# Kernel tuning notes

Measured on AMD Instinct MI355X. Metric: run time of the kernel, lower is better.

## Reference

```python
import jax, jax.numpy as jnp
from jax import lax
import numpy as np

N_QUBITS = 8
Q_DEPTH = 10
DIM = 256  # 2**8

# basis-state bit table; wire 0 = most-significant bit (PennyLane convention)
_bits = ((np.arange(DIM)[:, None] >> (N_QUBITS - 1 - np.arange(N_QUBITS))) & 1)
# phase layer: S on even wires (phase i), T on odd wires (phase e^{i pi/4})
_ph = np.where(np.arange(N_QUBITS) % 2 == 0, 1j, np.exp(1j * np.pi / 4))
_diag = np.prod(np.power(_ph[None, :], _bits), axis=1)
# entangling_layer_3 CZ pattern
_cz = np.ones(DIM)
for i, j in [(0, 1), (2, 3), (4, 5), (6, 7), (1, 2), (3, 4), (5, 6)]:
    _cz = _cz * ((-1.0) ** (_bits[:, i] * _bits[:, j]))
DIAG = jnp.asarray((_diag * _cz).astype(np.complex64))  # phase+CZ layer fused diagonal
ZSIGNS = jnp.asarray((1 - 2 * _bits).astype(np.float32))  # [256, 8] PauliZ eigenvalues
H_GATE = jnp.asarray((np.array([[1.0, 1.0], [1.0, -1.0]]) / np.sqrt(2.0)).astype(np.complex64))
X_GATE = jnp.asarray(np.array([[0.0, 1.0], [1.0, 0.0]]).astype(np.complex64))
EYE2 = jnp.eye(2, dtype=jnp.complex64)
BN_EPS = 1e-5


def apply_1q(state, U, w):
    """Apply 2x2 gate U on wire w; state: [B, 2,2,...,2]."""
    state = jnp.moveaxis(state, w + 1, -1)
    state = jnp.matmul(state, U.T)
    return jnp.moveaxis(state, -1, w + 1)


def quantum_net(features, q_params):
    """Batched statevector sim of quantum_net_3. features [B,256], q_params [80] -> [B,8]."""
    f = features / jnp.linalg.norm(features, axis=1, keepdims=True)
    state = f.astype(jnp.complex64).reshape((-1,) + (2,) * N_QUBITS)
    for w in range(N_QUBITS):
        state = apply_1q(state, H_GATE, w)
    qw = q_params.reshape(Q_DEPTH, N_QUBITS)
    for layer in range(Q_DEPTH):
        for w in range(N_QUBITS):
            t = qw[layer, w]
            c = jnp.cos(t / 2).astype(jnp.complex64)
            s = jnp.sin(t / 2).astype(jnp.complex64)
            U = c * EYE2 + (-1j) * s * X_GATE  # RX(t)
            state = apply_1q(state, U, w)
        flat = state.reshape(-1, DIM) * DIAG  # phase layer + CZ entangling (diagonal)
        state = flat.reshape((-1,) + (2,) * N_QUBITS)
    sv = state.reshape(-1, DIM)
    probs = sv.real ** 2 + sv.imag ** 2
    return probs @ ZSIGNS  # [B, 8] expval(PauliZ_i)


def conv2d(x, w, b):
    y = lax.conv_general_dilated(x, w, (1, 1), 'SAME', dimension_numbers=('NCHW', 'OIHW', 'NCHW'))
    return y + b[None, :, None, None]


def bn(x, gamma, beta, mean, var):  # eval-mode BatchNorm2d
    inv = gamma / jnp.sqrt(var + BN_EPS)
    return x * inv[None, :, None, None] + (beta - mean * inv)[None, :, None, None]


def maxpool2(x):
    return lax.reduce_window(x, -jnp.inf, lax.max, (1, 1, 2, 2), (1, 1, 2, 2), 'VALID')


def setup_inputs() -> dict:
    key = jax.random.key(0)
    ks = jax.random.split(key, 16)
    B = 1024
    return {
        'x': jax.random.normal(ks[0], (B, 1, 28, 28), dtype=jnp.float32),
        'conv1_w': 0.1 * jax.random.normal(ks[1], (32, 1, 3, 3), dtype=jnp.float32),
        'conv1_b': jnp.zeros((32,), jnp.float32),
        'bn1_gamma': jnp.ones((32,), jnp.float32),
        'bn1_beta': jnp.zeros((32,), jnp.float32),
        'bn1_mean': jnp.zeros((32,), jnp.float32),
        'bn1_var': jnp.ones((32,), jnp.float32),
        'conv2_w': 0.05 * jax.random.normal(ks[2], (64, 32, 3, 3), dtype=jnp.float32),
        'conv2_b': jnp.zeros((64,), jnp.float32),
        'bn2_gamma': jnp.ones((64,), jnp.float32),
        'bn2_beta': jnp.zeros((64,), jnp.float32),
        'bn2_mean': jnp.zeros((64,), jnp.float32),
        'bn2_var': jnp.ones((64,), jnp.float32),
        'fc_w': 0.01 * jax.random.normal(ks[3], (256, 64 * 7 * 7), dtype=jnp.float32),
        'fc_b': jnp.zeros((256,), jnp.float32),
        'q_params': 0.1 * jax.random.normal(ks[4], (Q_DEPTH * N_QUBITS,), dtype=jnp.float32),
        'p1_w': 0.01 * jax.random.normal(ks[5], (128, 8), dtype=jnp.float32),
        'p1_b': jnp.zeros((128,), jnp.float32),
        'p2_w': 0.01 * jax.random.normal(ks[6], (64, 128), dtype=jnp.float32),
        'p2_b': jnp.zeros((64,), jnp.float32),
        'p3_w': 0.01 * jax.random.normal(ks[7], (10, 64), dtype=jnp.float32),
        'p3_b': jnp.zeros((10,), jnp.float32),
    }


def reference(x, conv1_w, conv1_b, bn1_gamma, bn1_beta, bn1_mean, bn1_var,
              conv2_w, conv2_b, bn2_gamma, bn2_beta, bn2_mean, bn2_var,
              fc_w, fc_b, q_params, p1_w, p1_b, p2_w, p2_b, p3_w, p3_b):
    h = maxpool2(jax.nn.relu(bn(conv2d(x, conv1_w, conv1_b), bn1_gamma, bn1_beta, bn1_mean, bn1_var)))
    h = maxpool2(jax.nn.relu(bn(conv2d(h, conv2_w, conv2_b), bn2_gamma, bn2_beta, bn2_mean, bn2_var)))
    h = h.reshape(h.shape[0], -1)  # [B, 64*7*7]
    feats = jnp.tanh(h @ fc_w.T + fc_b)  # [B, 256]
    q = quantum_net(feats, q_params)  # [B, 8]
    z = jax.nn.relu(q @ p1_w.T + p1_b)  # dropout = identity (eval)
    z = jax.nn.relu(z @ p2_w.T + p2_b)
    return z @ p3_w.T + p3_b
```

## Files before the change

kernel.cpp:

```cpp
#include <hip/hip_runtime.h>
#include <math.h>


#define B_SZ 1024

#define OFF_FCWP   0
#define OFF_W2F    802816
#define OFF_W1T    821248
#define OFF_SC1    821536
#define OFF_SH1    821568
#define OFF_SC2    821600
#define OFF_SH2    821664
#define OFF_H1     821728
#define OFF_H2P    7244256

#define KSPLIT_FC 14
#define KCHUNK_FC 224

typedef __attribute__((ext_vector_type(8))) short s16x8;
typedef __attribute__((ext_vector_type(4))) float f32x4;

__constant__ float C_COS8[8] = {1.f, 0.70710678f, 0.f, -0.70710678f, -1.f, -0.70710678f, 0.f, 0.70710678f};
__constant__ float C_SIN8[8] = {0.f, 0.70710678f, 1.f, 0.70710678f, 0.f, -0.70710678f, -1.f, -0.70710678f};

__device__ __forceinline__ unsigned short bf16_rne(float f) {
  unsigned u = __float_as_uint(f);
  unsigned r = u + 0x7FFFu + ((u >> 16) & 1u);
  return (unsigned short)(r >> 16);
}
__device__ __forceinline__ int div14(int m) {
  return __float2int_rz((float)m * 0.07142858f);
}

__global__ __launch_bounds__(256) void prep_kernel(
    const float* __restrict__ fc_w, const float* __restrict__ c2w, const float* __restrict__ c1w,
    const float* __restrict__ bn1g, const float* __restrict__ bn1b, const float* __restrict__ bn1m,
    const float* __restrict__ bn1v, const float* __restrict__ c1b,
    const float* __restrict__ bn2g, const float* __restrict__ bn2b, const float* __restrict__ bn2m,
    const float* __restrict__ bn2v, const float* __restrict__ c2b,
    float* __restrict__ ws) {
  int g = blockIdx.x * 256 + threadIdx.x;

  {
    int j = g & 7, lane = (g >> 3) & 63, nt = (g >> 9) & 15, kg = g >> 13;
    int n = nt * 16 + (lane & 15);
    int k = kg * 32 + ((lane >> 4) & 3) * 8 + j;
    float v = fc_w[n * 3136 + (k & 63) * 49 + (k >> 6)];
    unsigned short hi = bf16_rne(v);
    unsigned short lo = bf16_rne(v - __uint_as_float((unsigned)hi << 16));
    unsigned short* us = (unsigned short*)ws;
    int base = ((kg * 16 + nt) * 2) * 512 + lane * 8 + j;
    us[base] = hi;
    us[base + 512] = lo;
  }

  if (g < 36864) {
    int j = g & 7, L = (g >> 3) & 63, rest = g >> 9;
    int h = rest & 1; rest >>= 1;
    int t = rest % 9, w = rest / 9;
    int occ = w * 16 + (L & 15);
    int ic  = (L >> 4) * 8 + j;
    float v = c2w[occ * 288 + ic * 9 + t];
    unsigned short hi = bf16_rne(v);
    unsigned short res = hi;
    if (h) res = bf16_rne(v - __uint_as_float((unsigned)hi << 16));
    ((unsigned short*)(ws + OFF_W2F))[g] = res;
  }
  if (g < 288) {
    ws[OFF_W1T + g] = c1w[(g & 31) * 9 + (g >> 5)];
  }
  if (g < 32) {
    float inv = bn1g[g] / sqrtf(bn1v[g] + 1e-5f);
    ws[OFF_SC1 + g] = inv;
    ws[OFF_SH1 + g] = c1b[g] * inv + bn1b[g] - bn1m[g] * inv;
  }
  if (g < 64) {
    float inv = bn2g[g] / sqrtf(bn2v[g] + 1e-5f);
    ws[OFF_SC2 + g] = inv;
    ws[OFF_SH2 + g] = c2b[g] * inv + bn2b[g] - bn2m[g] * inv;
  }
}

__global__ __launch_bounds__(256) void conv1_kernel(
    const float* __restrict__ x, const float* __restrict__ w1T,
    const float* __restrict__ sc1, const float* __restrict__ sh1,
    float* __restrict__ h1) {
  const int b = blockIdx.x, tid = threadIdx.x;
  __shared__ float xs[30][32];
  __shared__ float w1s[288];
  __shared__ float sc1s[32], sh1s[32];

  float4* xsf = (float4*)&xs[0][0];
  if (tid < 240) xsf[tid] = make_float4(0.f, 0.f, 0.f, 0.f);
  __syncthreads();
  const float* xb = x + b * 784;
  for (int i = tid; i < 784; i += 256) {
    int y = i / 28, c = i - y * 28;
    xs[y + 1][c + 1] = xb[i];
  }
  for (int i = tid; i < 288; i += 256) w1s[i] = w1T[i];
  if (tid < 32) { sc1s[tid] = sc1[tid]; sh1s[tid] = sh1[tid]; }
  __syncthreads();

  for (int t = tid; t < 448; t += 256) {
    const int oc = t & 31, py = t >> 5;
    float wv[9];
#pragma unroll
    for (int k = 0; k < 9; ++k) wv[k] = w1s[k * 32 + oc];
    float acc0[28], acc1[28];
#pragma unroll
    for (int j = 0; j < 28; ++j) { acc0[j] = 0.f; acc1[j] = 0.f; }
#pragma unroll
    for (int r = 0; r < 4; ++r) {
      const int pr = 2 * py + r;
      float row[32];
#pragma unroll
      for (int q = 0; q < 8; ++q) {
        float4 v = *(const float4*)&xs[pr][4 * q];
        row[4 * q] = v.x; row[4 * q + 1] = v.y; row[4 * q + 2] = v.z; row[4 * q + 3] = v.w;
      }
      if (r <= 2) {
#pragma unroll
        for (int kx = 0; kx < 3; ++kx) {
          const float w = wv[r * 3 + kx];
#pragma unroll
          for (int xx = 0; xx < 28; ++xx) acc0[xx] = fmaf(row[xx + kx], w, acc0[xx]);
        }
      }
      if (r >= 1) {
#pragma unroll
        for (int kx = 0; kx < 3; ++kx) {
          const float w = wv[(r - 1) * 3 + kx];
#pragma unroll
          for (int xx = 0; xx < 28; ++xx) acc1[xx] = fmaf(row[xx + kx], w, acc1[xx]);
        }
      }
    }
    const float sc = sc1s[oc], sh = sh1s[oc];
    float* dst = h1 + b * 6272 + oc * 196 + py * 14;
#pragma unroll
    for (int px = 0; px < 14; ++px) {
      float v0 = fmaxf(fmaf(acc0[2 * px], sc, sh), 0.f);
      float v1 = fmaxf(fmaf(acc0[2 * px + 1], sc, sh), 0.f);
      float v2 = fmaxf(fmaf(acc1[2 * px], sc, sh), 0.f);
      float v3 = fmaxf(fmaf(acc1[2 * px + 1], sc, sh), 0.f);
      dst[px] = fmaxf(fmaxf(v0, v1), fmaxf(v2, v3));
    }
  }
}

__global__ __launch_bounds__(256, 2) void conv2_kernel(
    const float* __restrict__ h1, const float* __restrict__ w2f_f,
    const float* __restrict__ sc2, const float* __restrict__ sh2,
    unsigned short* __restrict__ h2hi, unsigned short* __restrict__ h2lo) {
  const int b = blockIdx.x, tid = threadIdx.x;
  const int lane = tid & 63, w = tid >> 6;

  __shared__ unsigned char lds_raw[50176];
  unsigned short* tile_hi = (unsigned short*)lds_raw;
  unsigned short* tile_lo = (unsigned short*)(lds_raw + 17408);
  float* conv_out = (float*)lds_raw;

  const unsigned short* w2f = (const unsigned short*)w2f_f;
  s16x8 bf[9][2];
#pragma unroll
  for (int t = 0; t < 9; ++t)
#pragma unroll
    for (int h = 0; h < 2; ++h)
      bf[t][h] = *(const s16x8*)&w2f[(((w * 9 + t) * 2 + h) << 9) + lane * 8];

  {
    float4* z = (float4*)lds_raw;
    for (int i = tid; i < 2176; i += 256) z[i] = make_float4(0.f, 0.f, 0.f, 0.f);
  }
  __syncthreads();

  if (tid < 196) {
    const int y = div14(tid), x = tid - y * 14;
    const int sp = ((y + 1) * 16 + (x + 1)) * 32;
    const float* src = h1 + b * 6272 + tid;
#pragma unroll
    for (int c = 0; c < 4; ++c) {
      s16x8 hv, lv;
#pragma unroll
      for (int j = 0; j < 8; ++j) {
        float v = src[(c * 8 + j) * 196];
        unsigned short h16 = bf16_rne(v);
        hv[j] = (short)h16;
        lv[j] = (short)bf16_rne(v - __uint_as_float((unsigned)h16 << 16));
      }
      *(s16x8*)&tile_hi[sp + c * 8] = hv;
      *(s16x8*)&tile_lo[sp + c * 8] = lv;
    }
  }
  __syncthreads();

  f32x4 acc[13];
#pragma unroll
  for (int i = 0; i < 13; ++i) acc[i] = (f32x4){0.f, 0.f, 0.f, 0.f};

  const int kg8 = (lane >> 4) * 8;
#pragma unroll
  for (int mt = 0; mt < 13; ++mt) {
    const int m = mt * 16 + (lane & 15);
    const int y = div14(m), x = m - y * 14;
    const int base = (y * 16 + x) * 32 + kg8;
#pragma unroll
    for (int dy = 0; dy < 3; ++dy) {
#pragma unroll
      for (int dx = 0; dx < 3; ++dx) {
        const int off = base + (dy * 16 + dx) * 32;
        s16x8 ah = *(s16x8*)&tile_hi[off];
        s16x8 al = *(s16x8*)&tile_lo[off];
        const int t = dy * 3 + dx;
        acc[mt] = __builtin_amdgcn_mfma_f32_16x16x32_bf16(ah, bf[t][0], acc[mt], 0, 0, 0);
        acc[mt] = __builtin_amdgcn_mfma_f32_16x16x32_bf16(ah, bf[t][1], acc[mt], 0, 0, 0);
        acc[mt] = __builtin_amdgcn_mfma_f32_16x16x32_bf16(al, bf[t][0], acc[mt], 0, 0, 0);
      }
    }
  }
  __syncthreads();

  const int oc = w * 16 + (lane & 15);
  const float sc = sc2[oc], sh = sh2[oc];
  float* cw = conv_out + w * 3136;
#pragma unroll
  for (int mt = 0; mt < 13; ++mt) {
#pragma unroll
    for (int r = 0; r < 4; ++r) {
      const int m = mt * 16 + (lane >> 4) * 4 + r;
      if (m < 196) cw[m * 16 + (lane & 15)] = fmaxf(fmaf(acc[mt][r], sc, sh), 0.f);
    }
  }
  __syncthreads();

#pragma unroll
  for (int i = 0; i < 13; ++i) {
    const int ps = i * 4 + (lane >> 4);
    if (ps < 49) {
      const int py = (ps * 37) >> 8, px = ps - py * 7;
      const int m00 = py * 28 + px * 2;
      const int c0 = m00 * 16 + (lane & 15);
      float v0 = cw[c0], v1 = cw[c0 + 16], v2 = cw[c0 + 224], v3 = cw[c0 + 240];
      float vm = fmaxf(fmaxf(v0, v1), fmaxf(v2, v3));
      unsigned short hv = bf16_rne(vm);
      const int idx = b * 3136 + ps * 64 + oc;
      h2hi[idx] = hv;
      h2lo[idx] = bf16_rne(vm - __uint_as_float((unsigned)hv << 16));
    }
  }
}

__global__ __launch_bounds__(256) void fc_mfma_kernel(
    const unsigned short* __restrict__ h2hi, const unsigned short* __restrict__ h2lo,
    const unsigned short* __restrict__ Bfrag, float* __restrict__ Part) {
  __shared__ unsigned short Bs[8192];
  const int tid = threadIdx.x;
  const int lane = tid & 63, w = tid >> 6;
  const int m0 = blockIdx.y * 64, nt0 = blockIdx.x * 8, z = blockIdx.z;
  const int kz = z * KCHUNK_FC;

  const int mrow = m0 + w * 16 + (lane & 15);
  const int kg8 = (lane >> 4) * 8;
  const unsigned short* arow_hi = h2hi + mrow * 3136;
  const unsigned short* arow_lo = h2lo + mrow * 3136;

  f32x4 acc[8];
#pragma unroll
  for (int i = 0; i < 8; ++i) acc[i] = (f32x4){0.f, 0.f, 0.f, 0.f};

  for (int c = 0; c < 7; ++c) {
    const int kg = (kz >> 5) + c;
    {
      const uint4* src = (const uint4*)(Bfrag + (size_t)(kg * 16 + nt0) * 1024);
      uint4* dst = (uint4*)Bs;
#pragma unroll
      for (int i = 0; i < 4; ++i) dst[tid + 256 * i] = src[tid + 256 * i];
    }
    __syncthreads();

    const int k0 = kz + c * 32;
    s16x8 ah = *(const s16x8*)(arow_hi + k0 + kg8);
    s16x8 al = *(const s16x8*)(arow_lo + k0 + kg8);
#pragma unroll
    for (int nf = 0; nf < 8; ++nf) {
      s16x8 bh = *(s16x8*)&Bs[(nf * 2 + 0) * 512 + lane * 8];
      s16x8 bl = *(s16x8*)&Bs[(nf * 2 + 1) * 512 + lane * 8];
      acc[nf] = __builtin_amdgcn_mfma_f32_16x16x32_bf16(ah, bh, acc[nf], 0, 0, 0);
      acc[nf] = __builtin_amdgcn_mfma_f32_16x16x32_bf16(ah, bl, acc[nf], 0, 0, 0);
      acc[nf] = __builtin_amdgcn_mfma_f32_16x16x32_bf16(al, bh, acc[nf], 0, 0, 0);
    }
    __syncthreads();
  }

  float* dst = Part + (size_t)z * 262144;
  const int mbase = m0 + w * 16 + (lane >> 4) * 4;
  const int nbase = nt0 * 16 + (lane & 15);
#pragma unroll
  for (int nf = 0; nf < 8; ++nf) {
#pragma unroll
    for (int r = 0; r < 4; ++r) {
      dst[(mbase + r) * 256 + nbase + nf * 16] = acc[nf][r];
    }
  }
}

__global__ __launch_bounds__(256) void quantum_kernel(
    const float* __restrict__ Part, const float* __restrict__ fc_b,
    const float* __restrict__ qp,
    const float* __restrict__ p1w, const float* __restrict__ p1b,
    const float* __restrict__ p2w, const float* __restrict__ p2b,
    const float* __restrict__ p3w, const float* __restrict__ p3b,
    float* __restrict__ out) {
  const int b = blockIdx.x, tid = threadIdx.x;
  __shared__ float2 buf[2][256];
  __shared__ float csl[160];
  __shared__ float part[4][8];
  __shared__ float qv[8];
  __shared__ float z1[128];
  __shared__ float z2s[64];

  if (tid < 80) {
    float t = 0.5f * qp[tid];
    csl[2 * tid] = cosf(t);
    csl[2 * tid + 1] = sinf(t);
  }

  float f = fc_b[tid];
#pragma unroll
  for (int z = 0; z < KSPLIT_FC; ++z) f += Part[z * 262144 + b * 256 + tid];
  f = tanhf(f);

  float ss = f * f;
#pragma unroll
  for (int off = 32; off >= 1; off >>= 1) ss += __shfl_xor(ss, off);
  const int lane = tid & 63, wid = tid >> 6;
  if (lane == 0) part[wid][0] = ss;
  __syncthreads();
  const float tot = part[0][0] + part[1][0] + part[2][0] + part[3][0];
  const float inv = 1.0f / sqrtf(tot);
  float re = f * inv, im = 0.f;

  const int k8 = (2 * __popc(tid & 0xAA) + __popc(tid & 0x55)) & 7;
  float dre = C_COS8[k8], dim_ = C_SIN8[k8];
  {
    const int i = tid;
    int par = ((i >> 7) & (i >> 6)) ^ ((i >> 5) & (i >> 4)) ^ ((i >> 3) & (i >> 2)) ^ ((i >> 1) & i)
            ^ ((i >> 6) & (i >> 5)) ^ ((i >> 4) & (i >> 3)) ^ ((i >> 2) & (i >> 1));
    if (par & 1) { dre = -dre; dim_ = -dim_; }
  }

  int cur = 0;
  const float RS = 0.70710678118654752f;

#pragma unroll
  for (int w = 0; w < 2; ++w) {
    const int m = 128 >> w;
    cur ^= 1;
    buf[cur][tid] = make_float2(re, im);
    __syncthreads();
    float2 p = buf[cur][tid ^ m];
    float sgn = (tid & m) ? -1.f : 1.f;
    re = fmaf(sgn, re, p.x) * RS;
    im = fmaf(sgn, im, p.y) * RS;
  }
#pragma unroll
  for (int w = 2; w < 8; ++w) {
    const int m = 1 << (7 - w);
    float pre = __shfl_xor(re, m);
    float pim = __shfl_xor(im, m);
    float sgn = (tid & m) ? -1.f : 1.f;
    re = fmaf(sgn, re, pre) * RS;
    im = fmaf(sgn, im, pim) * RS;
  }

  for (int layer = 0; layer < 10; ++layer) {
    const float* cs = &csl[16 * layer];
#pragma unroll
    for (int w = 0; w < 2; ++w) {
      const int m = 128 >> w;
      const float c = cs[2 * w], s = cs[2 * w + 1];
      cur ^= 1;
      buf[cur][tid] = make_float2(re, im);
      __syncthreads();
      float2 p = buf[cur][tid ^ m];
      float nre = fmaf(s, p.y, c * re);
      float nim = fmaf(-s, p.x, c * im);
      re = nre; im = nim;
    }
#pragma unroll
    for (int w = 2; w < 8; ++w) {
      const int m = 1 << (7 - w);
      const float c = cs[2 * w], s = cs[2 * w + 1];
      float pre = __shfl_xor(re, m);
      float pim = __shfl_xor(im, m);
      float nre = fmaf(s, pim, c * re);
      float nim = fmaf(-s, pre, c * im);
      if (w == 7) {
        float tre = nre * dre - nim * dim_;
        nim = fmaf(nre, dim_, nim * dre);
        nre = tre;
      }
      re = nre; im = nim;
    }
  }

  const float prb = re * re + im * im;
#pragma unroll
  for (int w = 0; w < 8; ++w) {
    float v = ((tid >> (7 - w)) & 1) ? -prb : prb;
#pragma unroll
    for (int off = 32; off >= 1; off >>= 1) v += __shfl_xor(v, off);
    if (lane == 0) part[wid][w] = v;
  }
  __syncthreads();
  if (tid < 8) qv[tid] = part[0][tid] + part[1][tid] + part[2][tid] + part[3][tid];
  __syncthreads();

  if (tid < 128) {
    float a = p1b[tid];
#pragma unroll
    for (int k = 0; k < 8; ++k) a = fmaf(qv[k], p1w[tid * 8 + k], a);
    z1[tid] = fmaxf(a, 0.f);
  }
  __syncthreads();
  if (tid < 64) {
    float a = p2b[tid];
#pragma unroll 16
    for (int k = 0; k < 128; ++k) a = fmaf(z1[k], p2w[tid * 128 + k], a);
    z2s[tid] = fmaxf(a, 0.f);
  }
  __syncthreads();
  if (tid < 10) {
    float a = p3b[tid];
#pragma unroll 16
    for (int k = 0; k < 64; ++k) a = fmaf(z2s[k], p3w[tid * 64 + k], a);
    out[b * 10 + tid] = a;
  }
}

extern "C" void kernel_launch(void* const* d_in, const int* in_sizes, int n_in,
                              void* d_out, int out_size, void* d_ws, size_t ws_size,
                              hipStream_t stream) {
  (void)in_sizes; (void)n_in; (void)out_size; (void)ws_size;
  const float* x    = (const float*)d_in[0];
  const float* c1w  = (const float*)d_in[1];
  const float* c1b  = (const float*)d_in[2];
  const float* bn1g = (const float*)d_in[3];
  const float* bn1b = (const float*)d_in[4];
  const float* bn1m = (const float*)d_in[5];
  const float* bn1v = (const float*)d_in[6];
  const float* c2w  = (const float*)d_in[7];
  const float* c2b  = (const float*)d_in[8];
  const float* bn2g = (const float*)d_in[9];
  const float* bn2b = (const float*)d_in[10];
  const float* bn2m = (const float*)d_in[11];
  const float* bn2v = (const float*)d_in[12];
  const float* fc_w = (const float*)d_in[13];
  const float* fc_b = (const float*)d_in[14];
  const float* qp   = (const float*)d_in[15];
  const float* p1w  = (const float*)d_in[16];
  const float* p1b  = (const float*)d_in[17];
  const float* p2w  = (const float*)d_in[18];
  const float* p2b  = (const float*)d_in[19];
  const float* p3w  = (const float*)d_in[20];
  const float* p3b  = (const float*)d_in[21];
  float* ws = (float*)d_ws;
  float* outp = (float*)d_out;

  unsigned short* h2hi = (unsigned short*)(ws + OFF_H2P);
  unsigned short* h2lo = h2hi + 3211264;
  const unsigned short* bfrag = (const unsigned short*)ws;

  prep_kernel<<<3136, 256, 0, stream>>>(fc_w, c2w, c1w,
                                        bn1g, bn1b, bn1m, bn1v, c1b,
                                        bn2g, bn2b, bn2m, bn2v, c2b, ws);
  conv1_kernel<<<B_SZ, 256, 0, stream>>>(x, ws + OFF_W1T, ws + OFF_SC1, ws + OFF_SH1, ws + OFF_H1);
  conv2_kernel<<<B_SZ, 256, 0, stream>>>(ws + OFF_H1, ws + OFF_W2F, ws + OFF_SC2, ws + OFF_SH2,
                                         h2hi, h2lo);
  fc_mfma_kernel<<<dim3(2, 16, KSPLIT_FC), 256, 0, stream>>>(h2hi, h2lo, bfrag, ws + OFF_H1);
  quantum_kernel<<<B_SZ, 256, 0, stream>>>(ws + OFF_H1, fc_b, qp, p1w, p1b, p2w, p2b, p3w, p3b, outp);
}
```

Before: 177.6 us.

## Fuse prep into conv1 launch, pad conv2 LDS tile, drop LDS staging in FC

Merges the weight-prep and conv1 kernels into one launch, with extra blocks doing the fc/conv2 weight repacking and conv1 computing its BN scale/shift inline. The fc_w repack now reads rows coalesced through shared memory. Conv2's LDS tile stride is padded from 32 to 40 elements to cut bank conflicts. The FC kernel drops LDS staging and barriers, loads B fragments straight from global memory, and uses 4 n-tiles per block over a doubled grid. Risks include more global B traffic in FC and a race on ws: the prep blocks write weights into the same launch as conv1, so they must finish before conv2 reads them.

```diff
diff --git a/kernel.cpp b/kernel.cpp
--- a/kernel.cpp
+++ b/kernel.cpp
@@ -6,16 +6,13 @@
 
 #define OFF_FCWP   0
 #define OFF_W2F    802816
-#define OFF_W1T    821248
-#define OFF_SC1    821536
-#define OFF_SH1    821568
 #define OFF_SC2    821600
 #define OFF_SH2    821664
 #define OFF_H1     821728
 #define OFF_H2P    7244256
 
 #define KSPLIT_FC 14
-#define KCHUNK_FC 224
+#define TS 40
 
 typedef __attribute__((ext_vector_type(8))) short s16x8;
 typedef __attribute__((ext_vector_type(4))) float f32x4;
@@ -32,74 +29,77 @@
   return __float2int_rz((float)m * 0.07142858f);
 }
 
-__global__ __launch_bounds__(256) void prep_kernel(
-    const float* __restrict__ fc_w, const float* __restrict__ c2w, const float* __restrict__ c1w,
+__global__ __launch_bounds__(256) void fused_front_kernel(
+    const float* __restrict__ x, const float* __restrict__ c1w, const float* __restrict__ c1b,
     const float* __restrict__ bn1g, const float* __restrict__ bn1b, const float* __restrict__ bn1m,
-    const float* __restrict__ bn1v, const float* __restrict__ c1b,
+    const float* __restrict__ bn1v,
+    const float* __restrict__ c2w,
     const float* __restrict__ bn2g, const float* __restrict__ bn2b, const float* __restrict__ bn2m,
     const float* __restrict__ bn2v, const float* __restrict__ c2b,
+    const float* __restrict__ fc_w,
     float* __restrict__ ws) {
-  int g = blockIdx.x * 256 + threadIdx.x;
-
-  {
-    int j = g & 7, lane = (g >> 3) & 63, nt = (g >> 9) & 15, kg = g >> 13;
-    int n = nt * 16 + (lane & 15);
-    int k = kg * 32 + ((lane >> 4) & 3) * 8 + j;
-    float v = fc_w[n * 3136 + (k & 63) * 49 + (k >> 6)];
-    unsigned short hi = bf16_rne(v);
-    unsigned short lo = bf16_rne(v - __uint_as_float((unsigned)hi << 16));
-    unsigned short* us = (unsigned short*)ws;
-    int base = ((kg * 16 + nt) * 2) * 512 + lane * 8 + j;
-    us[base] = hi;
-    us[base + 512] = lo;
-  }
-
-  if (g < 36864) {
-    int j = g & 7, L = (g >> 3) & 63, rest = g >> 9;
-    int h = rest & 1; rest >>= 1;
-    int t = rest % 9, w = rest / 9;
-    int occ = w * 16 + (L & 15);
-    int ic  = (L >> 4) * 8 + j;
-    float v = c2w[occ * 288 + ic * 9 + t];
-    unsigned short hi = bf16_rne(v);
-    unsigned short res = hi;
-    if (h) res = bf16_rne(v - __uint_as_float((unsigned)hi << 16));
-    ((unsigned short*)(ws + OFF_W2F))[g] = res;
-  }
-  if (g < 288) {
-    ws[OFF_W1T + g] = c1w[(g & 31) * 9 + (g >> 5)];
-  }
-  if (g < 32) {
-    float inv = bn1g[g] / sqrtf(bn1v[g] + 1e-5f);
-    ws[OFF_SC1 + g] = inv;
-    ws[OFF_SH1 + g] = c1b[g] * inv + bn1b[g] - bn1m[g] * inv;
-  }
-  if (g < 64) {
-    float inv = bn2g[g] / sqrtf(bn2v[g] + 1e-5f);
-    ws[OFF_SC2 + g] = inv;
-    ws[OFF_SH2 + g] = c2b[g] * inv + bn2b[g] - bn2m[g] * inv;
-  }
-}
-
-__global__ __launch_bounds__(256) void conv1_kernel(
-    const float* __restrict__ x, const float* __restrict__ w1T,
-    const float* __restrict__ sc1, const float* __restrict__ sh1,
-    float* __restrict__ h1) {
-  const int b = blockIdx.x, tid = threadIdx.x;
-  __shared__ float xs[30][32];
-  __shared__ float w1s[288];
-  __shared__ float sc1s[32], sh1s[32];
-
-  float4* xsf = (float4*)&xs[0][0];
-  if (tid < 240) xsf[tid] = make_float4(0.f, 0.f, 0.f, 0.f);
+  const int blk = blockIdx.x, tid = threadIdx.x;
+  __shared__ float smem[3136];
+
+  if (blk >= 1024) {
+    if (blk < 1280) {
+      const int n = blk - 1024;
+      const float* src = fc_w + n * 3136;
+      for (int i = tid; i < 3136; i += 256) smem[i] = src[i];
+      __syncthreads();
+      unsigned short* us = (unsigned short*)ws;
+      const int nt = n >> 4, nl = n & 15;
+      for (int k = tid; k < 3136; k += 256) {
+        float v = smem[(k & 63) * 49 + (k >> 6)];
+        unsigned short hi = bf16_rne(v);
+        unsigned short lo = bf16_rne(v - __uint_as_float((unsigned)hi << 16));
+        const int lane_ = ((k >> 3) & 3) * 16 + nl;
+        const int base = (((k >> 5) * 16 + nt) * 2) * 512 + lane_ * 8 + (k & 7);
+        us[base] = hi;
+        us[base + 512] = lo;
+      }
+    } else if (blk < 1424) {
+      int g = (blk - 1280) * 256 + tid;
+      int j = g & 7, L = (g >> 3) & 63, rest = g >> 9;
+      int h = rest & 1; rest >>= 1;
+      int t = rest % 9, w = rest / 9;
+      int occ = w * 16 + (L & 15);
+      int ic  = (L >> 4) * 8 + j;
+      float v = c2w[occ * 288 + ic * 9 + t];
+      unsigned short hi = bf16_rne(v);
+      unsigned short res = hi;
+      if (h) res = bf16_rne(v - __uint_as_float((unsigned)hi << 16));
+      ((unsigned short*)(ws + OFF_W2F))[g] = res;
+    } else {
+      if (tid < 64) {
+        float inv = bn2g[tid] / sqrtf(bn2v[tid] + 1e-5f);
+        ws[OFF_SC2 + tid] = inv;
+        ws[OFF_SH2 + tid] = c2b[tid] * inv + bn2b[tid] - bn2m[tid] * inv;
+      }
+    }
+    return;
+  }
+
+  const int b = blk;
+  float (*xs)[32] = (float (*)[32])smem;
+  float* w1s  = smem + 960;
+  float* sc1s = smem + 1248;
+  float* sh1s = smem + 1280;
+  float* h1 = ws + OFF_H1;
+
+  if (tid < 240) ((float4*)smem)[tid] = make_float4(0.f, 0.f, 0.f, 0.f);
   __syncthreads();
   const float* xb = x + b * 784;
   for (int i = tid; i < 784; i += 256) {
     int y = i / 28, c = i - y * 28;
     xs[y + 1][c + 1] = xb[i];
   }
-  for (int i = tid; i < 288; i += 256) w1s[i] = w1T[i];
-  if (tid < 32) { sc1s[tid] = sc1[tid]; sh1s[tid] = sh1[tid]; }
+  for (int i = tid; i < 288; i += 256) w1s[i] = c1w[(i & 31) * 9 + (i >> 5)];
+  if (tid < 32) {
+    float inv = bn1g[tid] / sqrtf(bn1v[tid] + 1e-5f);
+    sc1s[tid] = inv;
+    sh1s[tid] = c1b[tid] * inv + bn1b[tid] - bn1m[tid] * inv;
+  }
   __syncthreads();
 
   for (int t = tid; t < 448; t += 256) {
@@ -158,7 +158,7 @@
 
   __shared__ unsigned char lds_raw[50176];
   unsigned short* tile_hi = (unsigned short*)lds_raw;
-  unsigned short* tile_lo = (unsigned short*)(lds_raw + 17408);
+  unsigned short* tile_lo = (unsigned short*)(lds_raw + 21760);
   float* conv_out = (float*)lds_raw;
 
   const unsigned short* w2f = (const unsigned short*)w2f_f;
@@ -171,13 +171,13 @@
 
   {
     float4* z = (float4*)lds_raw;
-    for (int i = tid; i < 2176; i += 256) z[i] = make_float4(0.f, 0.f, 0.f, 0.f);
+    for (int i = tid; i < 2720; i += 256) z[i] = make_float4(0.f, 0.f, 0.f, 0.f);
   }
   __syncthreads();
 
   if (tid < 196) {
     const int y = div14(tid), x = tid - y * 14;
-    const int sp = ((y + 1) * 16 + (x + 1)) * 32;
+    const int sp = ((y + 1) * 16 + (x + 1)) * TS;
     const float* src = h1 + b * 6272 + tid;
 #pragma unroll
     for (int c = 0; c < 4; ++c) {
@@ -204,12 +204,12 @@
   for (int mt = 0; mt < 13; ++mt) {
     const int m = mt * 16 + (lane & 15);
     const int y = div14(m), x = m - y * 14;
-    const int base = (y * 16 + x) * 32 + kg8;
+    const int base = (y * 16 + x) * TS + kg8;
 #pragma unroll
     for (int dy = 0; dy < 3; ++dy) {
 #pragma unroll
       for (int dx = 0; dx < 3; ++dx) {
-        const int off = base + (dy * 16 + dx) * 32;
+        const int off = base + (dy * 16 + dx) * TS;
         s16x8 ah = *(s16x8*)&tile_hi[off];
         s16x8 al = *(s16x8*)&tile_lo[off];
         const int t = dy * 3 + dx;
@@ -254,53 +254,42 @@
 __global__ __launch_bounds__(256) void fc_mfma_kernel(
     const unsigned short* __restrict__ h2hi, const unsigned short* __restrict__ h2lo,
     const unsigned short* __restrict__ Bfrag, float* __restrict__ Part) {
-  __shared__ unsigned short Bs[8192];
   const int tid = threadIdx.x;
   const int lane = tid & 63, w = tid >> 6;
-  const int m0 = blockIdx.y * 64, nt0 = blockIdx.x * 8, z = blockIdx.z;
-  const int kz = z * KCHUNK_FC;
-
-  const int mrow = m0 + w * 16 + (lane & 15);
+  const int nt0 = blockIdx.x * 4, z = blockIdx.z;
+  const int mrow = blockIdx.y * 64 + w * 16 + (lane & 15);
   const int kg8 = (lane >> 4) * 8;
-  const unsigned short* arow_hi = h2hi + mrow * 3136;
-  const unsigned short* arow_lo = h2lo + mrow * 3136;
-
-  f32x4 acc[8];
-#pragma unroll
-  for (int i = 0; i < 8; ++i) acc[i] = (f32x4){0.f, 0.f, 0.f, 0.f};
-
+  const unsigned short* arow_hi = h2hi + mrow * 3136 + kg8;
+  const unsigned short* arow_lo = h2lo + mrow * 3136 + kg8;
+
+  f32x4 acc[4];
+#pragma unroll
+  for (int i = 0; i < 4; ++i) acc[i] = (f32x4){0.f, 0.f, 0.f, 0.f};
+
+#pragma unroll
   for (int c = 0; c < 7; ++c) {
-    const int kg = (kz >> 5) + c;
-    {
-      const uint4* src = (const uint4*)(Bfrag + (size_t)(kg * 16 + nt0) * 1024);
-      uint4* dst = (uint4*)Bs;
-#pragma unroll
-      for (int i = 0; i < 4; ++i) dst[tid + 256 * i] = src[tid + 256 * i];
-    }
-    __syncthreads();
-
-    const int k0 = kz + c * 32;
-    s16x8 ah = *(const s16x8*)(arow_hi + k0 + kg8);
-    s16x8 al = *(const s16x8*)(arow_lo + k0 + kg8);
-#pragma unroll
-    for (int nf = 0; nf < 8; ++nf) {
-      s16x8 bh = *(s16x8*)&Bs[(nf * 2 + 0) * 512 + lane * 8];
-      s16x8 bl = *(s16x8*)&Bs[(nf * 2 + 1) * 512 + lane * 8];
+    const int kg = z * 7 + c;
+    s16x8 ah = *(const s16x8*)(arow_hi + kg * 32);
+    s16x8 al = *(const s16x8*)(arow_lo + kg * 32);
+#pragma unroll
+    for (int nf = 0; nf < 4; ++nf) {
+      const unsigned short* bp = Bfrag + (size_t)((kg * 16 + nt0 + nf) * 2) * 512 + lane * 8;
+      s16x8 bh = *(const s16x8*)bp;
+      s16x8 bl = *(const s16x8*)(bp + 512);
       acc[nf] = __builtin_amdgcn_mfma_f32_16x16x32_bf16(ah, bh, acc[nf], 0, 0, 0);
       acc[nf] = __builtin_amdgcn_mfma_f32_16x16x32_bf16(ah, bl, acc[nf], 0, 0, 0);
       acc[nf] = __builtin_amdgcn_mfma_f32_16x16x32_bf16(al, bh, acc[nf], 0, 0, 0);
     }
-    __syncthreads();
   }
 
   float* dst = Part + (size_t)z * 262144;
-  const int mbase = m0 + w * 16 + (lane >> 4) * 4;
-  const int nbase = nt0 * 16 + (lane & 15);
-#pragma unroll
-  for (int nf = 0; nf < 8; ++nf) {
+  const int mbase = blockIdx.y * 64 + w * 16 + (lane >> 4) * 4;
+  const int nbase = (lane & 15);
+#pragma unroll
+  for (int nf = 0; nf < 4; ++nf) {
 #pragma unroll
     for (int r = 0; r < 4; ++r) {
-      dst[(mbase + r) * 256 + nbase + nf * 16] = acc[nf][r];
+      dst[(mbase + r) * 256 + (nt0 + nf) * 16 + nbase] = acc[nf][r];
     }
   }
 }
@@ -472,12 +461,10 @@
   unsigned short* h2lo = h2hi + 3211264;
   const unsigned short* bfrag = (const unsigned short*)ws;
 
-  prep_kernel<<<3136, 256, 0, stream>>>(fc_w, c2w, c1w,
-                                        bn1g, bn1b, bn1m, bn1v, c1b,
-                                        bn2g, bn2b, bn2m, bn2v, c2b, ws);
-  conv1_kernel<<<B_SZ, 256, 0, stream>>>(x, ws + OFF_W1T, ws + OFF_SC1, ws + OFF_SH1, ws + OFF_H1);
+  fused_front_kernel<<<1425, 256, 0, stream>>>(x, c1w, c1b, bn1g, bn1b, bn1m, bn1v,
+                                               c2w, bn2g, bn2b, bn2m, bn2v, c2b, fc_w, ws);
   conv2_kernel<<<B_SZ, 256, 0, stream>>>(ws + OFF_H1, ws + OFF_W2F, ws + OFF_SC2, ws + OFF_SH2,
                                          h2hi, h2lo);
-  fc_mfma_kernel<<<dim3(2, 16, KSPLIT_FC), 256, 0, stream>>>(h2hi, h2lo, bfrag, ws + OFF_H1);
+  fc_mfma_kernel<<<dim3(4, 16, KSPLIT_FC), 256, 0, stream>>>(h2hi, h2lo, bfrag, ws + OFF_H1);
   quantum_kernel<<<B_SZ, 256, 0, stream>>>(ws + OFF_H1, fc_b, qp, p1w, p1b, p2w, p2b, p3w, p3b, outp);
 }
```

New measurement: 180.3 us. Within noise of the previous version (+1.5%).
